# Kernel optimization log

Hardware: AMD Instinct MI355X
Metric: run time of the kernel (lower is better)

## Reference

```python
import jax, jax.numpy as jnp
import numpy as np

N_NODES = 50000
N_EDGES = 800000
N_GRAPHS = 50
D_IN = 128
D_HID = 128
D_OUT = 10


def setup_inputs() -> dict:
    key = jax.random.key(0)
    ks = jax.random.split(key, 8)
    h = jax.random.normal(ks[0], (N_NODES, D_IN), dtype=jnp.float32)
    src = jax.random.randint(ks[1], (N_EDGES,), 0, N_NODES, dtype=jnp.int32)
    dst = jax.random.randint(ks[2], (N_EDGES,), 0, N_NODES, dtype=jnp.int32)
    graph_ids = jnp.sort(jax.random.randint(ks[3], (N_NODES,), 0, N_GRAPHS, dtype=jnp.int32))
    s = 1.0 / np.sqrt(D_HID)
    W1 = jax.random.normal(ks[4], (D_IN, D_HID), dtype=jnp.float32) * s
    W2 = jax.random.normal(ks[5], (D_HID, D_HID), dtype=jnp.float32) * s
    W3 = jax.random.normal(ks[6], (D_HID, D_HID), dtype=jnp.float32) * s
    Wm = jax.random.normal(ks[7], (D_HID, D_OUT), dtype=jnp.float32) * s
    return {
        "h": h, "src": src, "dst": dst, "graph_ids": graph_ids,
        "W1": W1, "b1": jnp.zeros((D_HID,), jnp.float32),
        "W2": W2, "b2": jnp.zeros((D_HID,), jnp.float32),
        "W3": W3, "b3": jnp.zeros((D_HID,), jnp.float32),
        "Wm": Wm, "bm": jnp.zeros((D_OUT,), jnp.float32),
    }


def _graph_conv(h, W, b, src, dst, norm_src, norm_dst):
    # DGL GraphConv, norm='both': out = D_dst^{-1/2} * A @ (D_src^{-1/2} * h) @ W + b
    m = (h * norm_src[:, None])[src]              # [E, d] gather (memory-bound)
    agg = jax.ops.segment_sum(m, dst, num_segments=N_NODES)  # [N, d] scatter-add
    return (agg * norm_dst[:, None]) @ W + b


def reference(h, src, dst, graph_ids, W1, b1, W2, b2, W3, b3, Wm, bm):
    ones_e = jnp.ones((N_EDGES,), jnp.float32)
    out_deg = jax.ops.segment_sum(ones_e, src, num_segments=N_NODES)
    in_deg = jax.ops.segment_sum(ones_e, dst, num_segments=N_NODES)
    norm_src = jnp.clip(out_deg, 1.0, None) ** -0.5
    norm_dst = jnp.clip(in_deg, 1.0, None) ** -0.5

    h = jax.nn.relu(_graph_conv(h, W1, b1, src, dst, norm_src, norm_dst))
    h = jax.nn.relu(_graph_conv(h, W2, b2, src, dst, norm_src, norm_dst))
    h = jax.nn.relu(_graph_conv(h, W3, b3, src, dst, norm_src, norm_dst))

    # mean-nodes readout per graph
    hg_sum = jax.ops.segment_sum(h, graph_ids, num_segments=N_GRAPHS)  # [G, d]
    cnt = jax.ops.segment_sum(jnp.ones((N_NODES,), jnp.float32), graph_ids, num_segments=N_GRAPHS)
    hg = hg_sum / jnp.clip(cnt, 1.0, None)[:, None]

    logits = hg @ Wm + bm                                 # [G, D_OUT]
    return jax.nn.log_softmax(logits, axis=0)             # faithful to dim=0 in source
```

## Files before the change

### kernel.cpp

```cpp
#include <hip/hip_runtime.h>

#define N_NODES 50000
#define N_EDGES 800000
#define N_GRAPHS 50
#define D 128
#define D_OUT 10
#define PLANE_F4 200000
#define NB 196
#define NBLK 196
#define LCOL_CAP 3072
#define AST 68
#define ZWORDS 50576

__global__ __launch_bounds__(256) void part_hist(const int* __restrict__ dst,
                                                 int* __restrict__ gh,
                                                 int* __restrict__ zbuf) {
    __shared__ int lh[NB];
    int tid = threadIdx.x, blk = blockIdx.x;
    int z = blk * 256 + tid;
    if (z < ZWORDS) zbuf[z] = 0;
    z += 50176;
    if (z < ZWORDS) zbuf[z] = 0;
    if (tid < NB) lh[tid] = 0;
    __syncthreads();
    int base = blk * 4096;
    #pragma unroll
    for (int j = 0; j < 16; j++) {
        int i = base + j * 256 + tid;
        if (i < N_EDGES) atomicAdd(&lh[dst[i] >> 8], 1);
    }
    __syncthreads();
    if (tid < NB) gh[tid * NBLK + blk] = lh[tid];
}

__global__ __launch_bounds__(1024) void part_scan(int* __restrict__ gh) {
    __shared__ int wsum[16];
    __shared__ int carry_s;
    const int N = NB * NBLK;
    int tid = threadIdx.x;
    int lane = tid & 63, wid = tid >> 6;
    if (tid == 0) carry_s = 0;
    __syncthreads();
    for (int base = 0; base < N; base += 4096) {
        int i0 = base + tid * 4;
        int v0 = (i0 + 0 < N) ? gh[i0 + 0] : 0;
        int v1 = (i0 + 1 < N) ? gh[i0 + 1] : 0;
        int v2 = (i0 + 2 < N) ? gh[i0 + 2] : 0;
        int v3 = (i0 + 3 < N) ? gh[i0 + 3] : 0;
        int s = v0 + v1 + v2 + v3;
        int x = s;
        #pragma unroll
        for (int d = 1; d < 64; d <<= 1) {
            int y = __shfl_up(x, d, 64);
            if (lane >= d) x += y;
        }
        if (lane == 63) wsum[wid] = x;
        __syncthreads();
        if (wid == 0) {
            int t = (lane < 16) ? wsum[lane] : 0;
            #pragma unroll
            for (int d = 1; d < 16; d <<= 1) {
                int y = __shfl_up(t, d, 64);
                if (lane >= d) t += y;
            }
            if (lane < 16) wsum[lane] = t;
        }
        __syncthreads();
        int woff = (wid == 0) ? 0 : wsum[wid - 1];
        int run = carry_s + woff + (x - s);
        if (i0 + 0 < N) gh[i0 + 0] = run; run += v0;
        if (i0 + 1 < N) gh[i0 + 1] = run; run += v1;
        if (i0 + 2 < N) gh[i0 + 2] = run; run += v2;
        if (i0 + 3 < N) gh[i0 + 3] = run; run += v3;
        __syncthreads();
        if (tid == 0) carry_s += wsum[15];
        __syncthreads();
    }
}

__global__ __launch_bounds__(256) void part_scatter(const int* __restrict__ src,
                                                    const int* __restrict__ dst,
                                                    const int* __restrict__ gh,
                                                    unsigned int* __restrict__ packed,
                                                    int* __restrict__ out_deg) {
    __shared__ int lc[NB];
    int tid = threadIdx.x, blk = blockIdx.x;
    if (tid < NB) lc[tid] = gh[tid * NBLK + blk];
    __syncthreads();
    int base = blk * 4096;
    #pragma unroll
    for (int j = 0; j < 16; j++) {
        int i = base + j * 256 + tid;
        if (i < N_EDGES) {
            int d = dst[i];
            int s = src[i];
            atomicAdd(&out_deg[s], 1);
            int p = atomicAdd(&lc[d >> 8], 1);
            packed[p] = ((unsigned int)(d & 255) << 16) | (unsigned int)s;
        }
    }
}

__global__ __launch_bounds__(256) void bucket_csr(const unsigned int* __restrict__ packed,
                                                  const int* __restrict__ gh,
                                                  unsigned short* __restrict__ col16,
                                                  int* __restrict__ row_ptr,
                                                  float* __restrict__ nd) {
    __shared__ unsigned int ep[8192];
    __shared__ unsigned short lcol[8192];
    __shared__ int hist[256], cur[256], wsum[4];
    int t = threadIdx.x, b = blockIdx.x;
    int nb = gh[b * NBLK];
    int ne = (b < NB - 1) ? gh[(b + 1) * NBLK] : N_EDGES;
    int cnt = ne - nb;
    if (cnt > 8192) cnt = 8192;
    hist[t] = 0;
    __syncthreads();
    for (int i = t; i < cnt; i += 256) {
        unsigned int e = packed[nb + i];
        ep[i] = e;
        atomicAdd(&hist[e >> 16], 1);
    }
    __syncthreads();
    int v = hist[t];
    int lane = t & 63, w = t >> 6;
    int x = v;
    #pragma unroll
    for (int d = 1; d < 64; d <<= 1) {
        int y = __shfl_up(x, d, 64);
        if (lane >= d) x += y;
    }
    if (lane == 63) wsum[w] = x;
    __syncthreads();
    int add = 0;
    #pragma unroll
    for (int i = 0; i < 4; i++) if (i < w) add += wsum[i];
    int excl = add + x - v;
    cur[t] = excl;
    int node = b * 256 + t;
    if (node < N_NODES) {
        row_ptr[node] = nb + excl;
        int id = v > 1 ? v : 1;
        nd[node] = 1.0f / sqrtf((float)id);
    }
    if (b == NB - 1 && t == 0) row_ptr[N_NODES] = N_EDGES;
    __syncthreads();
    for (int i = t; i < cnt; i += 256) {
        unsigned int e = ep[i];
        int p = atomicAdd(&cur[e >> 16], 1);
        lcol[p] = (unsigned short)(e & 0xFFFF);
    }
    __syncthreads();
    for (int i = t; i < cnt; i += 256) col16[nb + i] = lcol[i];
}

__global__ __launch_bounds__(256) void prescale_k(const float* __restrict__ h,
                                                  const int* __restrict__ out_deg,
                                                  float* __restrict__ out) {
    int i = blockIdx.x * 256 + threadIdx.x;
    if (i < N_NODES * 32) {
        int node = i >> 5;
        int kg = i & 31;
        float4 v = ((const float4*)h)[i];
        int od = out_deg[node];
        float s = 1.0f / sqrtf((float)(od > 1 ? od : 1));
        int p = kg >> 2, q = kg & 3;
        ((float4*)out)[p * PLANE_F4 + node * 4 + q] =
            make_float4(v.x * s, v.y * s, v.z * s, v.w * s);
    }
}

__global__ __launch_bounds__(256) void spmm_k(const float* __restrict__ x,
                                              const int* __restrict__ row_ptr,
                                              const unsigned short* __restrict__ col,
                                              const float* __restrict__ nd,
                                              float* __restrict__ out) {
    __shared__ unsigned short lcol[LCOL_CAP];
    int b = blockIdx.x;
    int slice = b & 7;
    int n0b = (b >> 3) * 64;
    int nendb = n0b + 64; if (nendb > N_NODES) nendb = N_NODES;
    int e0 = row_ptr[n0b];
    int e1 = row_ptr[nendb];
    int cnt = e1 - e0;
    int staged = cnt < LCOL_CAP ? cnt : LCOL_CAP;
    for (int j = threadIdx.x; j < staged; j += 256) lcol[j] = col[e0 + j];
    __syncthreads();

    int node = n0b + (threadIdx.x >> 2);
    if (node >= N_NODES) return;
    int q = threadIdx.x & 3;
    int s = row_ptr[node];
    int e = row_ptr[node + 1];
    const float4* xp = (const float4*)x + slice * PLANE_F4;
    float4 a0 = make_float4(0.f, 0.f, 0.f, 0.f);
    float4 a1 = make_float4(0.f, 0.f, 0.f, 0.f);
    float4 a2 = make_float4(0.f, 0.f, 0.f, 0.f);
    float4 a3 = make_float4(0.f, 0.f, 0.f, 0.f);

    if (e - e0 <= staged) {
        const unsigned short* lc = lcol + (s - e0);
        int n = e - s;
        int i = 0;
        for (; i + 8 <= n; i += 8) {
            int c0 = lc[i],     c1 = lc[i + 1], c2 = lc[i + 2], c3 = lc[i + 3];
            int c4 = lc[i + 4], c5 = lc[i + 5], c6 = lc[i + 6], c7 = lc[i + 7];
            float4 h0 = xp[c0 * 4 + q];
            float4 h1 = xp[c1 * 4 + q];
            float4 h2 = xp[c2 * 4 + q];
            float4 h3 = xp[c3 * 4 + q];
            float4 h4 = xp[c4 * 4 + q];
            float4 h5 = xp[c5 * 4 + q];
            float4 h6 = xp[c6 * 4 + q];
            float4 h7 = xp[c7 * 4 + q];
            a0.x += h0.x; a0.y += h0.y; a0.z += h0.z; a0.w += h0.w;
            a1.x += h1.x; a1.y += h1.y; a1.z += h1.z; a1.w += h1.w;
            a2.x += h2.x; a2.y += h2.y; a2.z += h2.z; a2.w += h2.w;
            a3.x += h3.x; a3.y += h3.y; a3.z += h3.z; a3.w += h3.w;
            a0.x += h4.x; a0.y += h4.y; a0.z += h4.z; a0.w += h4.w;
            a1.x += h5.x; a1.y += h5.y; a1.z += h5.z; a1.w += h5.w;
            a2.x += h6.x; a2.y += h6.y; a2.z += h6.z; a2.w += h6.w;
            a3.x += h7.x; a3.y += h7.y; a3.z += h7.z; a3.w += h7.w;
        }
        for (; i + 4 <= n; i += 4) {
            int c0 = lc[i], c1 = lc[i + 1], c2 = lc[i + 2], c3 = lc[i + 3];
            float4 h0 = xp[c0 * 4 + q];
            float4 h1 = xp[c1 * 4 + q];
            float4 h2 = xp[c2 * 4 + q];
            float4 h3 = xp[c3 * 4 + q];
            a0.x += h0.x; a0.y += h0.y; a0.z += h0.z; a0.w += h0.w;
            a1.x += h1.x; a1.y += h1.y; a1.z += h1.z; a1.w += h1.w;
            a2.x += h2.x; a2.y += h2.y; a2.z += h2.z; a2.w += h2.w;
            a3.x += h3.x; a3.y += h3.y; a3.z += h3.z; a3.w += h3.w;
        }
        for (; i < n; i++) {
            float4 hv = xp[lc[i] * 4 + q];
            a0.x += hv.x; a0.y += hv.y; a0.z += hv.z; a0.w += hv.w;
        }
    } else {
        int i = s;
        for (; i + 4 <= e; i += 4) {
            int c0 = col[i], c1 = col[i + 1], c2 = col[i + 2], c3 = col[i + 3];
            float4 h0 = xp[c0 * 4 + q];
            float4 h1 = xp[c1 * 4 + q];
            float4 h2 = xp[c2 * 4 + q];
            float4 h3 = xp[c3 * 4 + q];
            a0.x += h0.x; a0.y += h0.y; a0.z += h0.z; a0.w += h0.w;
            a1.x += h1.x; a1.y += h1.y; a1.z += h1.z; a1.w += h1.w;
            a2.x += h2.x; a2.y += h2.y; a2.z += h2.z; a2.w += h2.w;
            a3.x += h3.x; a3.y += h3.y; a3.z += h3.z; a3.w += h3.w;
        }
        for (; i < e; i++) {
            float4 hv = xp[col[i] * 4 + q];
            a0.x += hv.x; a0.y += hv.y; a0.z += hv.z; a0.w += hv.w;
        }
    }
    float ndv = nd[node];
    ((float4*)out)[slice * PLANE_F4 + node * 4 + q] =
        make_float4((a0.x + a1.x + a2.x + a3.x) * ndv,
                    (a0.y + a1.y + a2.y + a3.y) * ndv,
                    (a0.z + a1.z + a2.z + a3.z) * ndv,
                    (a0.w + a1.w + a2.w + a3.w) * ndv);
}

template <int MODE>
__global__ __launch_bounds__(128) void gemm_relu_k(const float* __restrict__ A,
                                                   const float* __restrict__ W,
                                                   const float* __restrict__ bias,
                                                   const int* __restrict__ odeg,
                                                   float* __restrict__ out) {
    __shared__ float As_t[128 * AST];
    int tid = threadIdx.x;
    int row0 = blockIdx.x * 64;
    const float4* A4 = (const float4*)A;
    const float4* W4 = (const float4*)W;

    #pragma unroll
    for (int it = 0; it < 16; it++) {
        int linear = it * 128 + tid;
        int p = linear >> 8;
        int rem = linear & 255;
        int r = rem >> 2;
        int q = rem & 3;
        int row = row0 + r;
        float4 a = (row < N_NODES) ? A4[p * PLANE_F4 + row * 4 + q]
                                   : make_float4(0.f, 0.f, 0.f, 0.f);
        int kb = p * 16 + q * 4;
        As_t[(kb + 0) * AST + r] = a.x;
        As_t[(kb + 1) * AST + r] = a.y;
        As_t[(kb + 2) * AST + r] = a.z;
        As_t[(kb + 3) * AST + r] = a.w;
    }
    __syncthreads();

    int tc = tid & 15;
    int tr = tid >> 4;
    float acc[8][8];
    #pragma unroll
    for (int r = 0; r < 8; r++)
        #pragma unroll
        for (int c = 0; c < 8; c++) acc[r][c] = 0.f;

    const float4* Wp = W4 + tc * 2;
    const float*  Ab = As_t + tr * 8;

    for (int k0 = 0; k0 < 128; k0 += 4) {
        float4 wv0[4], wv1[4], av0[4], av1[4];
        #pragma unroll
        for (int u = 0; u < 4; u++) {
            wv0[u] = Wp[(k0 + u) * 32];
            wv1[u] = Wp[(k0 + u) * 32 + 1];
        }
        #pragma unroll
        for (int u = 0; u < 4; u++) {
            av0[u] = *(const float4*)(Ab + (k0 + u) * AST);
            av1[u] = *(const float4*)(Ab + (k0 + u) * AST + 4);
        }
        #pragma unroll
        for (int u = 0; u < 4; u++) {
            float av[8] = {av0[u].x, av0[u].y, av0[u].z, av0[u].w,
                           av1[u].x, av1[u].y, av1[u].z, av1[u].w};
            float wv[8] = {wv0[u].x, wv0[u].y, wv0[u].z, wv0[u].w,
                           wv1[u].x, wv1[u].y, wv1[u].z, wv1[u].w};
            #pragma unroll
            for (int rr = 0; rr < 8; rr++)
                #pragma unroll
                for (int cc = 0; cc < 8; cc++)
                    acc[rr][cc] = fmaf(av[rr], wv[cc], acc[rr][cc]);
        }
    }

    float4 bv0 = ((const float4*)bias)[tc * 2];
    float4 bv1 = ((const float4*)bias)[tc * 2 + 1];
    #pragma unroll
    for (int rr = 0; rr < 8; rr++) {
        int row = row0 + tr * 8 + rr;
        if (row < N_NODES) {
            float4 o0, o1;
            o0.x = fmaxf(acc[rr][0] + bv0.x, 0.f);
            o0.y = fmaxf(acc[rr][1] + bv0.y, 0.f);
            o0.z = fmaxf(acc[rr][2] + bv0.z, 0.f);
            o0.w = fmaxf(acc[rr][3] + bv0.w, 0.f);
            o1.x = fmaxf(acc[rr][4] + bv1.x, 0.f);
            o1.y = fmaxf(acc[rr][5] + bv1.y, 0.f);
            o1.z = fmaxf(acc[rr][6] + bv1.z, 0.f);
            o1.w = fmaxf(acc[rr][7] + bv1.w, 0.f);
            if (MODE == 0) {
                int od = odeg[row];
                float s = 1.0f / sqrtf((float)(od > 1 ? od : 1));
                o0.x *= s; o0.y *= s; o0.z *= s; o0.w *= s;
                o1.x *= s; o1.y *= s; o1.z *= s; o1.w *= s;
                int p = tc >> 1;
                int q0 = (tc & 1) * 2;
                ((float4*)out)[p * PLANE_F4 + row * 4 + q0] = o0;
                ((float4*)out)[p * PLANE_F4 + row * 4 + q0 + 1] = o1;
            } else {
                ((float4*)out)[row * 32 + tc * 2] = o0;
                ((float4*)out)[row * 32 + tc * 2 + 1] = o1;
            }
        }
    }
}

__global__ __launch_bounds__(256) void proj_readout_k(const float* __restrict__ h,
                                                      const int* __restrict__ gid,
                                                      const float* __restrict__ Wm,
                                                      float* __restrict__ hgp,
                                                      int* __restrict__ gcnt) {
    __shared__ float Wmt[10 * 144];
    int tid = threadIdx.x;
    for (int i = tid; i < 1280; i += 256) {
        int k = i / 10, o = i % 10;
        Wmt[o * 144 + k + 4 * (k >> 5)] = Wm[i];
    }
    __syncthreads();

    int v = blockIdx.x * 64 + (tid >> 2);
    int quarter = tid & 3;
    int lane = tid & 63;

    float acc[D_OUT];
    #pragma unroll
    for (int o = 0; o < D_OUT; o++) acc[o] = 0.f;
    int g = -1;
    int cnt = 0;
    if (v < N_NODES) {
        g = gid[v];
        cnt = (quarter == 0) ? 1 : 0;
        const float4* h4 = (const float4*)h + v * 32 + quarter * 8;
        const float* wbase = Wmt + quarter * 36;
        #pragma unroll
        for (int kk = 0; kk < 8; kk++) {
            float4 hv = h4[kk];
            #pragma unroll
            for (int o = 0; o < D_OUT; o++) {
                float4 w = *(const float4*)(wbase + o * 144 + kk * 4);
                acc[o] += hv.x * w.x + hv.y * w.y + hv.z * w.z + hv.w * w.w;
            }
        }
    }

    #pragma unroll
    for (int d = 1; d < 64; d <<= 1) {
        int gp = __shfl_up(g, d, 64);
        int cp = __shfl_up(cnt, d, 64);
        bool take = (lane >= d) && (gp == g);
        #pragma unroll
        for (int o = 0; o < D_OUT; o++) {
            float ap = __shfl_up(acc[o], d, 64);
            if (take) acc[o] += ap;
        }
        if (take) cnt += cp;
    }
    int gn = __shfl_down(g, 1, 64);
    bool tail = (lane == 63) || (gn != g);
    if (tail && g >= 0) {
        #pragma unroll
        for (int o = 0; o < D_OUT; o++) atomicAdd(&hgp[g * D_OUT + o], acc[o]);
        if (cnt > 0) atomicAdd(&gcnt[g], cnt);
    }
}

__global__ __launch_bounds__(512) void final_k(const float* __restrict__ hgp,
                                               const int* __restrict__ gcnt,
                                               const float* __restrict__ bm,
                                               float* __restrict__ out) {
    __shared__ float lg[N_GRAPHS * D_OUT];
    __shared__ float colm[D_OUT], colls[D_OUT];
    int tid = threadIdx.x;
    if (tid < N_GRAPHS * D_OUT) {
        int g = tid / D_OUT, o = tid % D_OUT;
        float c = (float)gcnt[g];
        lg[tid] = hgp[tid] / (c > 1.f ? c : 1.f) + bm[o];
    }
    __syncthreads();
    if (tid < D_OUT) {
        float m = -1e30f;
        for (int g = 0; g < N_GRAPHS; g++) m = fmaxf(m, lg[g * D_OUT + tid]);
        float s = 0.f;
        for (int g = 0; g < N_GRAPHS; g++) s += expf(lg[g * D_OUT + tid] - m);
        colm[tid] = m; colls[tid] = logf(s);
    }
    __syncthreads();
    if (tid < N_GRAPHS * D_OUT) {
        int o = tid % D_OUT;
        out[tid] = lg[tid] - colm[o] - colls[o];
    }
}

extern "C" void kernel_launch(void* const* d_in, const int* in_sizes, int n_in,
                              void* d_out, int out_size, void* d_ws, size_t ws_size,
                              hipStream_t stream) {
    const float* h_in = (const float*)d_in[0];
    const int*   src  = (const int*)d_in[1];
    const int*   dst  = (const int*)d_in[2];
    const int*   gid  = (const int*)d_in[3];
    const float* W1 = (const float*)d_in[4];  const float* b1 = (const float*)d_in[5];
    const float* W2 = (const float*)d_in[6];  const float* b2 = (const float*)d_in[7];
    const float* W3 = (const float*)d_in[8];  const float* b3 = (const float*)d_in[9];
    const float* Wm = (const float*)d_in[10]; const float* bm = (const float*)d_in[11];

    char* ws = (char*)d_ws;
    int*            row_ptr = (int*)(ws + 0);
    unsigned short* col16   = (unsigned short*)(ws + 200032);
    float*          nd      = (float*)(ws + 1800032);
    int*            out_deg = (int*)(ws + 2000032);
    int*            gcnt    = (int*)(ws + 2200032);
    float*          hgp     = (float*)(ws + 2200288);
    int*            gh      = (int*)(ws + 2202464);
    float*          bufA    = (float*)(ws + 2356128);
    float*          bufB    = (float*)(ws + 27956128);
    unsigned int*   packed  = (unsigned int*)bufB;

    part_hist<<<NBLK, 256, 0, stream>>>(dst, gh, out_deg);
    part_scan<<<1, 1024, 0, stream>>>(gh);
    part_scatter<<<NBLK, 256, 0, stream>>>(src, dst, gh, packed, out_deg);
    bucket_csr<<<NB, 256, 0, stream>>>(packed, gh, col16, row_ptr, nd);
    prescale_k<<<6250, 256, 0, stream>>>(h_in, out_deg, bufA);

    spmm_k<<<6256, 256, 0, stream>>>(bufA, row_ptr, col16, nd, bufB);
    gemm_relu_k<0><<<782, 128, 0, stream>>>(bufB, W1, b1, out_deg, bufA);
    spmm_k<<<6256, 256, 0, stream>>>(bufA, row_ptr, col16, nd, bufB);
    gemm_relu_k<0><<<782, 128, 0, stream>>>(bufB, W2, b2, out_deg, bufA);
    spmm_k<<<6256, 256, 0, stream>>>(bufA, row_ptr, col16, nd, bufB);
    gemm_relu_k<1><<<782, 128, 0, stream>>>(bufB, W3, b3, out_deg, bufA);

    proj_readout_k<<<782, 256, 0, stream>>>(bufA, gid, Wm, hgp, gcnt);
    final_k<<<1, 512, 0, stream>>>(hgp, gcnt, bm, (float*)d_out);
}
```

Baseline: 442.7 us.

## Sort nodes by in-degree to balance SpMM wavefront work, drop LDS column staging

Builds a degree histogram in bucket_csr, scans it, and scatters node ids into a degree-sorted permutation. SpMM then processes nodes in permutation order so the threads in a wavefront have similar neighbor counts, which reduces divergence and tail imbalance. The shared-memory staging of column indices is removed and columns are read directly from global memory. In exchange, consecutive threads now touch scattered rows, so col, row_ptr and output accesses lose locality. Two small preprocessing kernels are also added.

```diff
diff --git a/kernel.cpp b/kernel.cpp
--- a/kernel.cpp
+++ b/kernel.cpp
@@ -8,9 +8,8 @@
 #define PLANE_F4 200000
 #define NB 196
 #define NBLK 196
-#define LCOL_CAP 3072
 #define AST 68
-#define ZWORDS 50576
+#define ZWORDS 50640
 
 __global__ __launch_bounds__(256) void part_hist(const int* __restrict__ dst,
                                                  int* __restrict__ gh,
@@ -105,7 +104,8 @@
                                                   const int* __restrict__ gh,
                                                   unsigned short* __restrict__ col16,
                                                   int* __restrict__ row_ptr,
-                                                  float* __restrict__ nd) {
+                                                  float* __restrict__ nd,
+                                                  int* __restrict__ dh) {
     __shared__ unsigned int ep[8192];
     __shared__ unsigned short lcol[8192];
     __shared__ int hist[256], cur[256], wsum[4];
@@ -142,6 +142,7 @@
         row_ptr[node] = nb + excl;
         int id = v > 1 ? v : 1;
         nd[node] = 1.0f / sqrtf((float)id);
+        atomicAdd(&dh[v < 63 ? v : 63], 1);
     }
     if (b == NB - 1 && t == 0) row_ptr[N_NODES] = N_EDGES;
     __syncthreads();
@@ -152,6 +153,30 @@
     }
     __syncthreads();
     for (int i = t; i < cnt; i += 256) col16[nb + i] = lcol[i];
+}
+
+__global__ void dsort_scan(int* __restrict__ dh) {
+    int t = threadIdx.x;
+    int v = dh[t];
+    int x = v;
+    #pragma unroll
+    for (int d = 1; d < 64; d <<= 1) {
+        int y = __shfl_up(x, d, 64);
+        if (t >= d) x += y;
+    }
+    dh[t] = x - v;
+}
+
+__global__ __launch_bounds__(256) void dsort_scatter(const int* __restrict__ row_ptr,
+                                                     int* __restrict__ cursor,
+                                                     int* __restrict__ perm) {
+    int n = blockIdx.x * 256 + threadIdx.x;
+    if (n < N_NODES) {
+        int deg = row_ptr[n + 1] - row_ptr[n];
+        int bin = deg < 63 ? deg : 63;
+        int pos = atomicAdd(&cursor[bin], 1);
+        perm[pos] = n;
+    }
 }
 
 __global__ __launch_bounds__(256) void prescale_k(const float* __restrict__ h,
@@ -174,21 +199,13 @@
                                               const int* __restrict__ row_ptr,
                                               const unsigned short* __restrict__ col,
                                               const float* __restrict__ nd,
+                                              const int* __restrict__ perm,
                                               float* __restrict__ out) {
-    __shared__ unsigned short lcol[LCOL_CAP];
     int b = blockIdx.x;
     int slice = b & 7;
-    int n0b = (b >> 3) * 64;
-    int nendb = n0b + 64; if (nendb > N_NODES) nendb = N_NODES;
-    int e0 = row_ptr[n0b];
-    int e1 = row_ptr[nendb];
-    int cnt = e1 - e0;
-    int staged = cnt < LCOL_CAP ? cnt : LCOL_CAP;
-    for (int j = threadIdx.x; j < staged; j += 256) lcol[j] = col[e0 + j];
-    __syncthreads();
-
-    int node = n0b + (threadIdx.x >> 2);
-    if (node >= N_NODES) return;
+    int idx = (b >> 3) * 64 + (threadIdx.x >> 2);
+    if (idx >= N_NODES) return;
+    int node = perm[idx];
     int q = threadIdx.x & 3;
     int s = row_ptr[node];
     int e = row_ptr[node + 1];
@@ -197,63 +214,41 @@
     float4 a1 = make_float4(0.f, 0.f, 0.f, 0.f);
     float4 a2 = make_float4(0.f, 0.f, 0.f, 0.f);
     float4 a3 = make_float4(0.f, 0.f, 0.f, 0.f);
-
-    if (e - e0 <= staged) {
-        const unsigned short* lc = lcol + (s - e0);
-        int n = e - s;
-        int i = 0;
-        for (; i + 8 <= n; i += 8) {
-            int c0 = lc[i],     c1 = lc[i + 1], c2 = lc[i + 2], c3 = lc[i + 3];
-            int c4 = lc[i + 4], c5 = lc[i + 5], c6 = lc[i + 6], c7 = lc[i + 7];
-            float4 h0 = xp[c0 * 4 + q];
-            float4 h1 = xp[c1 * 4 + q];
-            float4 h2 = xp[c2 * 4 + q];
-            float4 h3 = xp[c3 * 4 + q];
-            float4 h4 = xp[c4 * 4 + q];
-            float4 h5 = xp[c5 * 4 + q];
-            float4 h6 = xp[c6 * 4 + q];
-            float4 h7 = xp[c7 * 4 + q];
-            a0.x += h0.x; a0.y += h0.y; a0.z += h0.z; a0.w += h0.w;
-            a1.x += h1.x; a1.y += h1.y; a1.z += h1.z; a1.w += h1.w;
-            a2.x += h2.x; a2.y += h2.y; a2.z += h2.z; a2.w += h2.w;
-            a3.x += h3.x; a3.y += h3.y; a3.z += h3.z; a3.w += h3.w;
-            a0.x += h4.x; a0.y += h4.y; a0.z += h4.z; a0.w += h4.w;
-            a1.x += h5.x; a1.y += h5.y; a1.z += h5.z; a1.w += h5.w;
-            a2.x += h6.x; a2.y += h6.y; a2.z += h6.z; a2.w += h6.w;
-            a3.x += h7.x; a3.y += h7.y; a3.z += h7.z; a3.w += h7.w;
-        }
-        for (; i + 4 <= n; i += 4) {
-            int c0 = lc[i], c1 = lc[i + 1], c2 = lc[i + 2], c3 = lc[i + 3];
-            float4 h0 = xp[c0 * 4 + q];
-            float4 h1 = xp[c1 * 4 + q];
-            float4 h2 = xp[c2 * 4 + q];
-            float4 h3 = xp[c3 * 4 + q];
-            a0.x += h0.x; a0.y += h0.y; a0.z += h0.z; a0.w += h0.w;
-            a1.x += h1.x; a1.y += h1.y; a1.z += h1.z; a1.w += h1.w;
-            a2.x += h2.x; a2.y += h2.y; a2.z += h2.z; a2.w += h2.w;
-            a3.x += h3.x; a3.y += h3.y; a3.z += h3.z; a3.w += h3.w;
-        }
-        for (; i < n; i++) {
-            float4 hv = xp[lc[i] * 4 + q];
-            a0.x += hv.x; a0.y += hv.y; a0.z += hv.z; a0.w += hv.w;
-        }
-    } else {
-        int i = s;
-        for (; i + 4 <= e; i += 4) {
-            int c0 = col[i], c1 = col[i + 1], c2 = col[i + 2], c3 = col[i + 3];
-            float4 h0 = xp[c0 * 4 + q];
-            float4 h1 = xp[c1 * 4 + q];
-            float4 h2 = xp[c2 * 4 + q];
-            float4 h3 = xp[c3 * 4 + q];
-            a0.x += h0.x; a0.y += h0.y; a0.z += h0.z; a0.w += h0.w;
-            a1.x += h1.x; a1.y += h1.y; a1.z += h1.z; a1.w += h1.w;
-            a2.x += h2.x; a2.y += h2.y; a2.z += h2.z; a2.w += h2.w;
-            a3.x += h3.x; a3.y += h3.y; a3.z += h3.z; a3.w += h3.w;
-        }
-        for (; i < e; i++) {
-            float4 hv = xp[col[i] * 4 + q];
-            a0.x += hv.x; a0.y += hv.y; a0.z += hv.z; a0.w += hv.w;
-        }
+    int i = s;
+    for (; i + 8 <= e; i += 8) {
+        int c0 = col[i],     c1 = col[i + 1], c2 = col[i + 2], c3 = col[i + 3];
+        int c4 = col[i + 4], c5 = col[i + 5], c6 = col[i + 6], c7 = col[i + 7];
+        float4 h0 = xp[c0 * 4 + q];
+        float4 h1 = xp[c1 * 4 + q];
+        float4 h2 = xp[c2 * 4 + q];
+        float4 h3 = xp[c3 * 4 + q];
+        float4 h4 = xp[c4 * 4 + q];
+        float4 h5 = xp[c5 * 4 + q];
+        float4 h6 = xp[c6 * 4 + q];
+        float4 h7 = xp[c7 * 4 + q];
+        a0.x += h0.x; a0.y += h0.y; a0.z += h0.z; a0.w += h0.w;
+        a1.x += h1.x; a1.y += h1.y; a1.z += h1.z; a1.w += h1.w;
+        a2.x += h2.x; a2.y += h2.y; a2.z += h2.z; a2.w += h2.w;
+        a3.x += h3.x; a3.y += h3.y; a3.z += h3.z; a3.w += h3.w;
+        a0.x += h4.x; a0.y += h4.y; a0.z += h4.z; a0.w += h4.w;
+        a1.x += h5.x; a1.y += h5.y; a1.z += h5.z; a1.w += h5.w;
+        a2.x += h6.x; a2.y += h6.y; a2.z += h6.z; a2.w += h6.w;
+        a3.x += h7.x; a3.y += h7.y; a3.z += h7.z; a3.w += h7.w;
+    }
+    for (; i + 4 <= e; i += 4) {
+        int c0 = col[i], c1 = col[i + 1], c2 = col[i + 2], c3 = col[i + 3];
+        float4 h0 = xp[c0 * 4 + q];
+        float4 h1 = xp[c1 * 4 + q];
+        float4 h2 = xp[c2 * 4 + q];
+        float4 h3 = xp[c3 * 4 + q];
+        a0.x += h0.x; a0.y += h0.y; a0.z += h0.z; a0.w += h0.w;
+        a1.x += h1.x; a1.y += h1.y; a1.z += h1.z; a1.w += h1.w;
+        a2.x += h2.x; a2.y += h2.y; a2.z += h2.z; a2.w += h2.w;
+        a3.x += h3.x; a3.y += h3.y; a3.z += h3.z; a3.w += h3.w;
+    }
+    for (; i < e; i++) {
+        float4 hv = xp[col[i] * 4 + q];
+        a0.x += hv.x; a0.y += hv.y; a0.z += hv.z; a0.w += hv.w;
     }
     float ndv = nd[node];
     ((float4*)out)[slice * PLANE_F4 + node * 4 + q] =
@@ -467,22 +462,26 @@
     int*            out_deg = (int*)(ws + 2000032);
     int*            gcnt    = (int*)(ws + 2200032);
     float*          hgp     = (float*)(ws + 2200288);
-    int*            gh      = (int*)(ws + 2202464);
-    float*          bufA    = (float*)(ws + 2356128);
-    float*          bufB    = (float*)(ws + 27956128);
+    int*            dh      = (int*)(ws + 2202336);
+    int*            gh      = (int*)(ws + 2202592);
+    int*            perm    = (int*)(ws + 2356256);
+    float*          bufA    = (float*)(ws + 2556256);
+    float*          bufB    = (float*)(ws + 28156256);
     unsigned int*   packed  = (unsigned int*)bufB;
 
     part_hist<<<NBLK, 256, 0, stream>>>(dst, gh, out_deg);
     part_scan<<<1, 1024, 0, stream>>>(gh);
     part_scatter<<<NBLK, 256, 0, stream>>>(src, dst, gh, packed, out_deg);
-    bucket_csr<<<NB, 256, 0, stream>>>(packed, gh, col16, row_ptr, nd);
+    bucket_csr<<<NB, 256, 0, stream>>>(packed, gh, col16, row_ptr, nd, dh);
+    dsort_scan<<<1, 64, 0, stream>>>(dh);
+    dsort_scatter<<<196, 256, 0, stream>>>(row_ptr, dh, perm);
     prescale_k<<<6250, 256, 0, stream>>>(h_in, out_deg, bufA);
 
-    spmm_k<<<6256, 256, 0, stream>>>(bufA, row_ptr, col16, nd, bufB);
+    spmm_k<<<6256, 256, 0, stream>>>(bufA, row_ptr, col16, nd, perm, bufB);
     gemm_relu_k<0><<<782, 128, 0, stream>>>(bufB, W1, b1, out_deg, bufA);
-    spmm_k<<<6256, 256, 0, stream>>>(bufA, row_ptr, col16, nd, bufB);
+    spmm_k<<<6256, 256, 0, stream>>>(bufA, row_ptr, col16, nd, perm, bufB);
     gemm_relu_k<0><<<782, 128, 0, stream>>>(bufB, W2, b2, out_deg, bufA);
-    spmm_k<<<6256, 256, 0, stream>>>(bufA, row_ptr, col16, nd, bufB);
+    spmm_k<<<6256, 256, 0, stream>>>(bufA, row_ptr, col16, nd, perm, bufB);
     gemm_relu_k<1><<<782, 128, 0, stream>>>(bufB, W3, b3, out_deg, bufA);
 
     proj_readout_k<<<782, 256, 0, stream>>>(bufA, gid, Wm, hgp, gcnt);
```

After: 803.7 us. 81.6% more time.
